# Kernel optimization log

Measured on AMD Instinct MI355X. Metric: run time of the kernel, lower is better.

Reference implementation:

```python
import jax, jax.numpy as jnp
import numpy as np

HIDDEN = 3072
HEADS = 24
HEAD_DIM = HIDDEN // HEADS  # 128
MLP_HIDDEN = 4 * HIDDEN     # 12288
EPS = 1e-6


def rotate_half(x):
    # interleaved pairs: (x1, x2) -> (-x2, x1)
    xr = x.reshape(*x.shape[:-1], -1, 2)
    x1, x2 = xr[..., 0], xr[..., 1]
    return jnp.stack((-x2, x1), axis=-1).reshape(x.shape)


def rms_norm(x, gamma):
    var = jnp.mean(x * x, axis=-1, keepdims=True)
    return x * jax.lax.rsqrt(var + EPS) * gamma


def layer_norm(x):
    mu = jnp.mean(x, axis=-1, keepdims=True)
    var = jnp.mean(jnp.square(x - mu), axis=-1, keepdims=True)
    return (x - mu) * jax.lax.rsqrt(var + EPS)


def setup_inputs() -> dict:
    key = jax.random.key(0)
    ks = jax.random.split(key, 8)
    B, L_IMG, TXT = 2, 1024, 256
    L = L_IMG + TXT
    s = 0.02
    x = jax.random.normal(ks[0], (B, L, HIDDEN), jnp.float32)
    vec = jax.random.normal(ks[1], (B, HIDDEN), jnp.float32)
    w1 = jax.random.normal(ks[2], (HIDDEN, 3 * HIDDEN + MLP_HIDDEN), jnp.float32) * s
    b1 = jnp.zeros((3 * HIDDEN + MLP_HIDDEN,), jnp.float32)
    w2 = jax.random.normal(ks[3], (HIDDEN + MLP_HIDDEN, HIDDEN), jnp.float32) * s
    b2 = jnp.zeros((HIDDEN,), jnp.float32)
    wmod = jax.random.normal(ks[4], (HIDDEN, 3 * HIDDEN), jnp.float32) * s
    bmod = jnp.zeros((3 * HIDDEN,), jnp.float32)
    q_gamma = jnp.ones((HEAD_DIM,), jnp.float32)
    k_gamma = jnp.ones((HEAD_DIM,), jnp.float32)
    # real RoPE tables for the image tokens
    inv_freq = 1.0 / (10000.0 ** (np.arange(0, HEAD_DIM, 2, dtype=np.float32) / HEAD_DIM))
    angles = np.arange(L_IMG, dtype=np.float32)[:, None] * inv_freq[None, :]  # [L_img, D/2]
    freqs_cos = jnp.asarray(np.repeat(np.cos(angles), 2, axis=-1))  # [L_img, D]
    freqs_sin = jnp.asarray(np.repeat(np.sin(angles), 2, axis=-1))
    cu_seqlens_q = jnp.asarray([0, L, L, 2 * L, 2 * L], jnp.int32)  # no padding
    return {"x": x, "vec": vec, "w1": w1, "b1": b1, "w2": w2, "b2": b2,
            "wmod": wmod, "bmod": bmod, "q_gamma": q_gamma, "k_gamma": k_gamma,
            "freqs_cos": freqs_cos, "freqs_sin": freqs_sin,
            "txt_len": TXT, "cu_seqlens_q": cu_seqlens_q}


def reference(x, vec, w1, b1, w2, b2, wmod, bmod, q_gamma, k_gamma,
              freqs_cos, freqs_sin, txt_len, cu_seqlens_q):
    B, L, _ = x.shape
    # modulation: SiLU(vec) @ Wmod -> shift/scale/gate
    mod = jax.nn.silu(vec) @ wmod + bmod              # [B, 3H]
    mod_shift, mod_scale, mod_gate = jnp.split(mod, 3, axis=-1)
    x_mod = layer_norm(x) * (1.0 + mod_scale[:, None, :]) + mod_shift[:, None, :]
    h = x_mod @ w1 + b1                               # [B, L, 3H + mlp]
    qkv, mlp = h[..., :3 * HIDDEN], h[..., 3 * HIDDEN:]
    qkv = qkv.reshape(B, L, 3, HEADS, HEAD_DIM)
    q, k, v = qkv[:, :, 0], qkv[:, :, 1], qkv[:, :, 2]  # [B, L, H, D]
    q = rms_norm(q, q_gamma)
    k = rms_norm(k, k_gamma)
    # RoPE on image tokens (first L - txt_len)
    cos = freqs_cos[None, :, None, :]
    sin = freqs_sin[None, :, None, :]
    img_q, txt_q = q[:, :-txt_len], q[:, -txt_len:]
    img_k, txt_k = k[:, :-txt_len], k[:, -txt_len:]
    img_q = img_q * cos + rotate_half(img_q) * sin
    img_k = img_k * cos + rotate_half(img_k) * sin
    q = jnp.concatenate((img_q, txt_q), axis=1)
    k = jnp.concatenate((img_k, txt_k), axis=1)
    # full attention (no padding => each batch is one varlen segment)
    scale = HEAD_DIM ** -0.5
    scores = jnp.einsum("bqhd,bkhd->bhqk", q, k) * scale
    probs = jax.nn.softmax(scores, axis=-1)
    attn = jnp.einsum("bhqk,bkhd->bqhd", probs, v).reshape(B, L, HIDDEN)
    out = jnp.concatenate((attn, jax.nn.gelu(mlp, approximate=True)), axis=-1) @ w2 + b2
    return x + out * mod_gate[:, None, :]
```

## Files before the change

### kernel.cpp

```cpp
#include <hip/hip_runtime.h>

typedef unsigned short u16;
typedef unsigned int   u32;
typedef __attribute__((ext_vector_type(2))) u16 u16x2;
typedef __attribute__((ext_vector_type(4))) u16 u16x4;
typedef __attribute__((ext_vector_type(8))) u16 u16x8;
typedef __attribute__((ext_vector_type(8))) __bf16 bf16x8;
typedef __attribute__((ext_vector_type(4))) float f32x4;

#define HIDDEN 3072
#define LTOT 1280
#define BATCH 2
#define NROWS (BATCH*LTOT)
#define HEADS 24
#define HD 128
#define N1 21504
#define QKVW 9216
#define MLPW 12288
#define A2W 15360
#define EPSF 1e-6f

__device__ __forceinline__ float b2f(u16 u) {
  union { u32 i; float f; } v; v.i = ((u32)u) << 16; return v.f;
}
__device__ __forceinline__ u16 f2b(float f) {
  union { float f; u32 i; } v; v.f = f;
  u32 r = (v.i + 0x7FFFu + ((v.i >> 16) & 1u)) >> 16;
  return (u16)r;
}
__device__ __forceinline__ float lde(const void* p, size_t i, int f) {
  return f ? b2f(((const u16*)p)[i]) : ((const float*)p)[i];
}
__device__ __forceinline__ void gload16(const void* g, void* l) {
  __builtin_amdgcn_global_load_lds((const __attribute__((address_space(1))) void*)g,
                                   (__attribute__((address_space(3))) void*)l, 16, 0, 0);
}
__device__ __forceinline__ float gelu_tanh(float x) {
  float u = 0.7978845608028654f * (x + 0.044715f * x * x * x);
  float e = __expf(2.0f * u);
  float th = 1.0f - 2.0f / (e + 1.0f);
  return 0.5f * x * (1.0f + th);
}

__global__ void detect_kernel(const u16* __restrict__ fcos, int* __restrict__ dflag) {
  if (threadIdx.x == 0 && blockIdx.x == 0) *dflag = (fcos[0] == 0x3F80) ? 1 : 0;
}

__global__ void silu_kernel(const void* __restrict__ vec, float* __restrict__ sv,
                            const int* __restrict__ dflag) {
  int flag = *dflag;
  int i = blockIdx.x * 256 + threadIdx.x;
  if (i < BATCH * HIDDEN) { float x = lde(vec, i, flag); sv[i] = x / (1.0f + __expf(-x)); }
}

__global__ void modmul(const void* __restrict__ wmod, const float* __restrict__ sv,
                       float* __restrict__ modp, const int* __restrict__ dflag) {
  int flag = *dflag;
  int j = blockIdx.x * 256 + threadIdx.x;
  int kc = blockIdx.y;
  float a = 0.f, c = 0.f;
  int k0 = kc * 384;
  for (int k = k0; k < k0 + 384; ++k) {
    float w = lde(wmod, (size_t)k * QKVW + j, flag);
    a += sv[k] * w; c += sv[HIDDEN + k] * w;
  }
  modp[(size_t)kc * 2 * QKVW + j] = a;
  modp[(size_t)kc * 2 * QKVW + QKVW + j] = c;
}

__global__ void modred(const float* __restrict__ modp, const void* __restrict__ bmod,
                       float* __restrict__ mod, const int* __restrict__ dflag) {
  int flag = *dflag;
  int j = blockIdx.x * 256 + threadIdx.x;
  float bv = lde(bmod, j, flag);
  float a = bv, c = bv;
#pragma unroll
  for (int kc = 0; kc < 8; ++kc) {
    a += modp[(size_t)kc * 2 * QKVW + j];
    c += modp[(size_t)kc * 2 * QKVW + QKVW + j];
  }
  mod[j] = a; mod[QKVW + j] = c;
}

__global__ __launch_bounds__(256) void ln_mod_kernel(const void* __restrict__ x,
                                                     const float* __restrict__ mod,
                                                     u16* __restrict__ xmod,
                                                     const int* __restrict__ dflag) {
  int flag = *dflag;
  int row = blockIdx.x;
  int b = row / LTOT;
  int t = threadIdx.x, w = t >> 6, l = t & 63;
  float v[12], sum = 0.0f, sq = 0.0f;
  if (flag) {
    const u16* xr = (const u16*)x + (size_t)row * HIDDEN;
#pragma unroll
    for (int p = 0; p < 3; ++p) {
      u16x4 u = *(const u16x4*)&xr[p * 1024 + t * 4];
#pragma unroll
      for (int i = 0; i < 4; ++i) { float f = b2f(u[i]); v[p * 4 + i] = f; sum += f; sq += f * f; }
    }
  } else {
    const float* xr = (const float*)x + (size_t)row * HIDDEN;
#pragma unroll
    for (int p = 0; p < 3; ++p) {
      f32x4 u = *(const f32x4*)&xr[p * 1024 + t * 4];
#pragma unroll
      for (int i = 0; i < 4; ++i) { float f = u[i]; v[p * 4 + i] = f; sum += f; sq += f * f; }
    }
  }
#pragma unroll
  for (int off = 1; off < 64; off <<= 1) { sum += __shfl_xor(sum, off, 64); sq += __shfl_xor(sq, off, 64); }
  __shared__ float red[2][4];
  if (l == 0) { red[0][w] = sum; red[1][w] = sq; }
  __syncthreads();
  sum = red[0][0] + red[0][1] + red[0][2] + red[0][3];
  sq  = red[1][0] + red[1][1] + red[1][2] + red[1][3];
  float mu = sum / (float)HIDDEN;
  float var = sq / (float)HIDDEN - mu * mu;
  float rs = rsqrtf(var + EPSF);
  const float* mb = mod + (size_t)b * QKVW;
#pragma unroll
  for (int p = 0; p < 3; ++p) {
    u16x4 o;
#pragma unroll
    for (int i = 0; i < 4; ++i) {
      int col = p * 1024 + t * 4 + i;
      float y = (v[p * 4 + i] - mu) * rs;
      o[i] = f2b(y * (1.0f + mb[HIDDEN + col]) + mb[col]);
    }
    *(u16x4*)&xmod[(size_t)row * HIDDEN + p * 1024 + t * 4] = o;
  }
}

__global__ void transpose_cvt(const void* __restrict__ in, u16* __restrict__ out,
                              int R, int C, const int* __restrict__ dflag) {
  int flag = *dflag;
  __shared__ u16 tile[32][33];
  int bx = blockIdx.x * 32, by = blockIdx.y * 32;
  int tx = threadIdx.x & 31, ty = threadIdx.x >> 5;
#pragma unroll
  for (int i = 0; i < 32; i += 8)
    tile[ty + i][tx] = f2b(lde(in, (size_t)(by + ty + i) * C + bx + tx, flag));
  __syncthreads();
#pragma unroll
  for (int i = 0; i < 32; i += 8) out[(size_t)(bx + ty + i) * R + by + tx] = tile[tx][ty + i];
}

__global__ void transpose_bf16(const u16* __restrict__ in, u16* __restrict__ out,
                               int R, int C, size_t ibs, size_t obs) {
  in  += (size_t)blockIdx.z * ibs;
  out += (size_t)blockIdx.z * obs;
  __shared__ u16 tile[32][33];
  int bx = blockIdx.x * 32, by = blockIdx.y * 32;
  int tx = threadIdx.x & 31, ty = threadIdx.x >> 5;
#pragma unroll
  for (int i = 0; i < 32; i += 8) tile[ty + i][tx] = in[(size_t)(by + ty + i) * C + bx + tx];
  __syncthreads();
#pragma unroll
  for (int i = 0; i < 32; i += 8) out[(size_t)(bx + ty + i) * R + by + tx] = tile[tx][ty + i];
}

template <int MODE>
__global__ __launch_bounds__(256) void gemm_bt(
    const u16* __restrict__ A, const u16* __restrict__ Bt, int K,
    const void* __restrict__ bias,
    u16* __restrict__ out0, u16* __restrict__ out1, u16* __restrict__ out2,
    u16* __restrict__ out3, float* __restrict__ outf,
    const void* __restrict__ xin, const float* __restrict__ mod,
    const int* __restrict__ dflag) {
  __shared__ u16 As[128 * 32];
  __shared__ u16 Bs[128 * 32];
  const int flag = *dflag;
  const int t = threadIdx.x;
  const int bn = blockIdx.x * 128;
  const int bm = blockIdx.y * 128;
  const int w = t >> 6, l = t & 63;
  const int wr = (w >> 1) * 64, wc = (w & 1) * 64;
  const int lr = l & 15, lk = (l >> 4) * 8;
  f32x4 acc[4][4] = {};
  const size_t a_base = (size_t)bm * K;
  const size_t b_base = (size_t)bn * K;
  const int e0 = t * 8, e1 = e0 + 2048;
  const int r0 = e0 >> 5, c0 = e0 & 31;
  const int r1 = e1 >> 5, c1 = e1 & 31;
  const int nk = K / 32;
  for (int kt = 0; kt < nk; ++kt) {
    const int k0 = kt * 32;
    __syncthreads();
    gload16(A + a_base + (size_t)r0 * K + k0 + c0, (u16*)As + e0);
    gload16(A + a_base + (size_t)r1 * K + k0 + c1, (u16*)As + e1);
    gload16(Bt + b_base + (size_t)r0 * K + k0 + c0, (u16*)Bs + e0);
    gload16(Bt + b_base + (size_t)r1 * K + k0 + c1, (u16*)Bs + e1);
    __syncthreads();
    bf16x8 af[4], bfr[4];
#pragma unroll
    for (int i = 0; i < 4; ++i) {
      af[i]  = __builtin_bit_cast(bf16x8, *(const u16x8*)&As[(wr + i * 16 + lr) * 32 + lk]);
      bfr[i] = __builtin_bit_cast(bf16x8, *(const u16x8*)&Bs[(wc + i * 16 + lr) * 32 + lk]);
    }
#pragma unroll
    for (int i = 0; i < 4; ++i)
#pragma unroll
      for (int j = 0; j < 4; ++j)
        acc[i][j] = __builtin_amdgcn_mfma_f32_16x16x32_bf16(af[i], bfr[j], acc[i][j], 0, 0, 0);
  }
#pragma unroll
  for (int i = 0; i < 4; ++i) {
#pragma unroll
    for (int j = 0; j < 4; ++j) {
      int colg = bn + wc + j * 16 + lr;
      float bv = lde(bias, colg, flag);
#pragma unroll
      for (int r = 0; r < 4; ++r) {
        int rowg = bm + wr + i * 16 + (l >> 4) * 4 + r;
        float v = acc[i][j][r] + bv;
        if (MODE == 1) {
          if (colg < QKVW) {
            int which = colg / HIDDEN;
            int hd = colg - which * HIDDEN;
            int h = hd >> 7, d = hd & 127;
            int b = rowg / LTOT, pos = rowg - b * LTOT;
            u16* dst = (which == 0) ? out0 : ((which == 1) ? out1 : out2);
            dst[(((size_t)(b * HEADS + h)) * LTOT + pos) * HD + d] = f2b(v);
          } else {
            out3[(size_t)rowg * A2W + HIDDEN + (colg - QKVW)] = f2b(gelu_tanh(v));
          }
        } else {
          int b = rowg / LTOT;
          float g = mod[(size_t)b * QKVW + 2 * HIDDEN + colg];
          float xv = lde(xin, (size_t)rowg * HIDDEN + colg, flag);
          outf[(size_t)rowg * HIDDEN + colg] = xv + v * g;
        }
      }
    }
  }
}

__global__ __launch_bounds__(256) void rms_rope(
    u16* __restrict__ Qb, u16* __restrict__ Kb,
    const void* __restrict__ qg, const void* __restrict__ kg,
    const void* __restrict__ fcos, const void* __restrict__ fsin,
    const int* __restrict__ dflag) {
  int flag = *dflag;
  int w = threadIdx.x >> 6, l = threadIdx.x & 63;
  int rid = blockIdx.x * 4 + w;
  int pos = rid % LTOT;
  int d0 = 2 * l;
  size_t off = (size_t)rid * HD + d0;
  u16x2 qu = *(const u16x2*)&Qb[off];
  u16x2 ku = *(const u16x2*)&Kb[off];
  float q0 = b2f(qu[0]), q1 = b2f(qu[1]);
  float k0 = b2f(ku[0]), k1 = b2f(ku[1]);
  float sq = q0 * q0 + q1 * q1, sk = k0 * k0 + k1 * k1;
#pragma unroll
  for (int o = 1; o < 64; o <<= 1) { sq += __shfl_xor(sq, o, 64); sk += __shfl_xor(sk, o, 64); }
  float rq = rsqrtf(sq / 128.0f + EPSF), rk = rsqrtf(sk / 128.0f + EPSF);
  q0 *= rq * lde(qg, d0, flag); q1 *= rq * lde(qg, d0 + 1, flag);
  k0 *= rk * lde(kg, d0, flag); k1 *= rk * lde(kg, d0 + 1, flag);
  if (pos < 1024) {
    float cc = lde(fcos, (size_t)pos * HD + d0, flag);
    float ss = lde(fsin, (size_t)pos * HD + d0, flag);
    float nq0 = q0 * cc - q1 * ss, nq1 = q1 * cc + q0 * ss;
    float nk0 = k0 * cc - k1 * ss, nk1 = k1 * cc + k0 * ss;
    q0 = nq0; q1 = nq1; k0 = nk0; k1 = nk1;
  }
  u16x2 qo; qo[0] = f2b(q0); qo[1] = f2b(q1);
  u16x2 ko; ko[0] = f2b(k0); ko[1] = f2b(k1);
  *(u16x2*)&Qb[off] = qo;
  *(u16x2*)&Kb[off] = ko;
}

__global__ __launch_bounds__(256) void attn_kernel(
    const u16* __restrict__ Qb, const u16* __restrict__ Kb, const u16* __restrict__ Vt,
    u16* __restrict__ A2) {
  __shared__ u16 Ks[32 * 128];
  __shared__ u16 Vs[128 * 32];
  __shared__ u16 Ps[4][512];
  int t = threadIdx.x, w = t >> 6, l = t & 63;
  int bh = blockIdx.y;
  int q0 = blockIdx.x * 64 + w * 16;
  size_t base = (size_t)bh * LTOT * HD;
  int lr = l & 15, lk = (l >> 4) * 8;
  const float scale = 0.08838834764831845f;

  bf16x8 qf[4];
#pragma unroll
  for (int c = 0; c < 4; ++c)
    qf[c] = __builtin_bit_cast(bf16x8, *(const u16x8*)&Qb[base + (size_t)(q0 + lr) * HD + c * 32 + lk]);

  f32x4 o[8] = {};
  float mrun[4] = {-1e30f, -1e30f, -1e30f, -1e30f};
  float lrun[4] = {0.f, 0.f, 0.f, 0.f};

  const int e0 = t * 8, e1 = e0 + 2048;
  const int vd0 = e0 >> 5, vc0 = e0 & 31;
  const int vd1 = e1 >> 5, vc1 = e1 & 31;

  for (int kt = 0; kt < LTOT / 32; ++kt) {
    __syncthreads();
    gload16(Kb + base + (size_t)kt * 32 * HD + e0, (u16*)Ks + e0);
    gload16(Kb + base + (size_t)kt * 32 * HD + e1, (u16*)Ks + e1);
    gload16(Vt + base + (size_t)vd0 * LTOT + kt * 32 + vc0, (u16*)Vs + e0);
    gload16(Vt + base + (size_t)vd1 * LTOT + kt * 32 + vc1, (u16*)Vs + e1);
    __syncthreads();

    f32x4 s[2] = {};
#pragma unroll
    for (int sb = 0; sb < 2; ++sb)
#pragma unroll
      for (int c = 0; c < 4; ++c) {
        bf16x8 kf = __builtin_bit_cast(bf16x8, *(const u16x8*)&Ks[(sb * 16 + lr) * 128 + c * 32 + lk]);
        s[sb] = __builtin_amdgcn_mfma_f32_16x16x32_bf16(qf[c], kf, s[sb], 0, 0, 0);
      }
#pragma unroll
    for (int sb = 0; sb < 2; ++sb)
#pragma unroll
      for (int j = 0; j < 4; ++j) s[sb][j] *= scale;

#pragma unroll
    for (int j = 0; j < 4; ++j) {
      float mt = fmaxf(s[0][j], s[1][j]);
#pragma unroll
      for (int off = 1; off < 16; off <<= 1) mt = fmaxf(mt, __shfl_xor(mt, off, 64));
      float mnew = fmaxf(mrun[j], mt);
      float f = __expf(mrun[j] - mnew);
      float p0 = __expf(s[0][j] - mnew), p1 = __expf(s[1][j] - mnew);
      float ps = p0 + p1;
#pragma unroll
      for (int off = 1; off < 16; off <<= 1) ps += __shfl_xor(ps, off, 64);
      lrun[j] = lrun[j] * f + ps;
      mrun[j] = mnew;
#pragma unroll
      for (int nb = 0; nb < 8; ++nb) o[nb][j] *= f;
      int prow = (l >> 4) * 4 + j;
      Ps[w][prow * 32 + lr] = f2b(p0);
      Ps[w][prow * 32 + 16 + lr] = f2b(p1);
    }
    __syncthreads();
    bf16x8 pa = __builtin_bit_cast(bf16x8, *(const u16x8*)&Ps[w][lr * 32 + lk]);
#pragma unroll
    for (int nb = 0; nb < 8; ++nb) {
      bf16x8 vf = __builtin_bit_cast(bf16x8, *(const u16x8*)&Vs[(nb * 16 + lr) * 32 + lk]);
      o[nb] = __builtin_amdgcn_mfma_f32_16x16x32_bf16(pa, vf, o[nb], 0, 0, 0);
    }
  }

  int b = bh / HEADS, h = bh % HEADS;
#pragma unroll
  for (int j = 0; j < 4; ++j) {
    float inv = 1.0f / lrun[j];
    size_t row = (size_t)b * LTOT + q0 + (l >> 4) * 4 + j;
#pragma unroll
    for (int nb = 0; nb < 8; ++nb) {
      int col = h * HD + nb * 16 + lr;
      A2[row * A2W + col] = f2b(o[nb][j] * inv);
    }
  }
}

extern "C" void kernel_launch(void* const* d_in, const int* in_sizes, int n_in,
                              void* d_out, int out_size, void* d_ws, size_t ws_size,
                              hipStream_t stream) {
  const void* x    = d_in[0];
  const void* vec  = d_in[1];
  const void* w1   = d_in[2];
  const void* b1   = d_in[3];
  const void* w2   = d_in[4];
  const void* b2   = d_in[5];
  const void* wmod = d_in[6];
  const void* bmod = d_in[7];
  const void* qg   = d_in[8];
  const void* kg   = d_in[9];
  const void* fcos = d_in[10];
  const void* fsin = d_in[11];

  char* p = (char*)d_ws;
  int* dflag  = (int*)p; p += 256;
  float* sv   = (float*)p; p += 32768;
  float* mod  = (float*)p; p += 131072;
  float* modp = (float*)p; p += 8 * 2 * QKVW * 4;
  u16* xmod = (u16*)p; p += (size_t)NROWS * HIDDEN * 2;
  u16* w1t  = (u16*)p; p += (size_t)N1 * HIDDEN * 2;
  u16* Qb   = (u16*)p; p += (size_t)48 * LTOT * HD * 2;
  u16* Kb   = (u16*)p; p += (size_t)48 * LTOT * HD * 2;
  u16* Vb   = (u16*)p; p += (size_t)48 * LTOT * HD * 2;
  u16* Vt   = (u16*)p; p += (size_t)48 * LTOT * HD * 2;
  u16* A2   = (u16*)p; p += (size_t)NROWS * A2W * 2;
  u16* w2t  = w1t;

  detect_kernel<<<1, 64, 0, stream>>>((const u16*)fcos, dflag);
  silu_kernel<<<24, 256, 0, stream>>>(vec, sv, dflag);
  modmul<<<dim3(36, 8), 256, 0, stream>>>(wmod, sv, modp, dflag);
  modred<<<36, 256, 0, stream>>>(modp, bmod, mod, dflag);
  ln_mod_kernel<<<NROWS, 256, 0, stream>>>(x, mod, xmod, dflag);
  transpose_cvt<<<dim3(N1 / 32, HIDDEN / 32), 256, 0, stream>>>(w1, w1t, HIDDEN, N1, dflag);
  gemm_bt<1><<<dim3(N1 / 128, NROWS / 128), 256, 0, stream>>>(xmod, w1t, HIDDEN, b1,
                                                              Qb, Kb, Vb, A2, nullptr,
                                                              nullptr, nullptr, dflag);
  rms_rope<<<48 * LTOT / 4, 256, 0, stream>>>(Qb, Kb, qg, kg, fcos, fsin, dflag);
  transpose_bf16<<<dim3(HD / 32, LTOT / 32, 48), 256, 0, stream>>>(Vb, Vt, LTOT, HD,
                                                                   (size_t)LTOT * HD, (size_t)LTOT * HD);
  attn_kernel<<<dim3(LTOT / 64, 48), 256, 0, stream>>>(Qb, Kb, Vt, A2);
  transpose_cvt<<<dim3(HIDDEN / 32, A2W / 32), 256, 0, stream>>>(w2, w2t, A2W, HIDDEN, dflag);
  gemm_bt<2><<<dim3(HIDDEN / 128, NROWS / 128), 256, 0, stream>>>(A2, w2t, A2W, b2,
                                                                  nullptr, nullptr, nullptr, nullptr,
                                                                  (float*)d_out, x, mod, dflag);
}
```

Baseline: 1.512 ms.

## Replace first GEMM with 256x256-tile, 512-thread double-buffered swizzled kernel

Adds a dedicated kernel for the large first projection GEMM. It uses 256x256 output tiles with 8 waves and double-buffered LDS filled by direct global-to-LDS loads. Reads use an XOR-swizzled LDS layout to avoid bank conflicts, MFMA sections are raised in priority with s_setprio, and workgroup IDs are remapped across XCDs for better L2 locality. The larger per-wave accumulator tile raises register pressure and cuts the number of workgroups, which risks lower occupancy and tail imbalance. The old MODE 1 epilogue in the generic GEMM is removed.

```diff
diff --git a/kernel.cpp b/kernel.cpp
--- a/kernel.cpp
+++ b/kernel.cpp
@@ -35,6 +35,9 @@
   __builtin_amdgcn_global_load_lds((const __attribute__((address_space(1))) void*)g,
                                    (__attribute__((address_space(3))) void*)l, 16, 0, 0);
 }
+__device__ __forceinline__ bf16x8 ldf(const u16* p) {
+  return __builtin_bit_cast(bf16x8, *(const u16x8*)p);
+}
 __device__ __forceinline__ float gelu_tanh(float x) {
   float u = 0.7978845608028654f * (x + 0.044715f * x * x * x);
   float e = __expf(2.0f * u);
@@ -158,6 +161,127 @@
   __syncthreads();
 #pragma unroll
   for (int i = 0; i < 32; i += 8) out[(size_t)(bx + ty + i) * R + by + tx] = tile[tx][ty + i];
+}
+
+__global__ __launch_bounds__(512, 2) void gemm1_8ph(
+    const u16* __restrict__ A, const u16* __restrict__ Bt,
+    const void* __restrict__ bias,
+    u16* __restrict__ Qb, u16* __restrict__ Kb, u16* __restrict__ Vb,
+    u16* __restrict__ A2, const int* __restrict__ dflag) {
+  __shared__ u16 As[2][2][256][32];
+  __shared__ u16 Bs[2][2][256][32];
+  constexpr int K = HIDDEN;
+  constexpr int NT = K / 64;
+  const int tid = threadIdx.x;
+  const int l = tid & 63, w = tid >> 6;
+  const int wr = w >> 2, wc = w & 3;
+  const int lr = l & 15, g = l >> 4;
+  const int lk_sw = (g ^ ((lr >> 1) & 3)) * 8;
+
+  const int orig = blockIdx.x;
+  const int wgid = (orig & 7) * 105 + (orig >> 3);
+  const int my = wgid / 84, nx = wgid - my * 84;
+  const int bm = my * 256, bn = nx * 256;
+
+  const int row_s = tid >> 2, chunk = tid & 3;
+  const int c_log = chunk ^ ((row_s >> 1) & 3);
+  const u16* pa = A  + (size_t)(bm + row_s) * K + c_log * 8;
+  const u16* pb = Bt + (size_t)(bn + row_s) * K + c_log * 8;
+
+  auto stage = [&](int buf, int kk, int t) {
+    const u16* sa = pa + kk * 32 + t * 64;
+    const u16* sb = pb + kk * 32 + t * 64;
+    u16* la = &As[buf][kk][row_s][chunk * 8];
+    u16* lb = &Bs[buf][kk][row_s][chunk * 8];
+    gload16(sa,                  la);
+    gload16(sa + (size_t)128 * K, la + 128 * 32);
+    gload16(sb,                  lb);
+    gload16(sb + (size_t)128 * K, lb + 128 * 32);
+  };
+
+  f32x4 acc[8][4] = {};
+  stage(0, 0, 0);
+  stage(0, 1, 0);
+
+  for (int t = 0; t < NT; ++t) {
+    const int buf = t & 1;
+    const bool pre = (t + 1 < NT);
+    asm volatile("s_waitcnt vmcnt(4)" ::: "memory");
+    __builtin_amdgcn_s_barrier();
+    __builtin_amdgcn_sched_barrier(0);
+    if (pre) stage(buf ^ 1, 0, t + 1);
+    bf16x8 bfr[4], af[4];
+#pragma unroll
+    for (int fc = 0; fc < 4; ++fc) bfr[fc] = ldf(&Bs[buf][0][wc * 64 + fc * 16 + lr][lk_sw]);
+#pragma unroll
+    for (int j = 0; j < 4; ++j) af[j] = ldf(&As[buf][0][wr * 128 + j * 16 + lr][lk_sw]);
+    __builtin_amdgcn_s_setprio(1);
+#pragma unroll
+    for (int j = 0; j < 4; ++j)
+#pragma unroll
+      for (int fc = 0; fc < 4; ++fc)
+        acc[j][fc] = __builtin_amdgcn_mfma_f32_16x16x32_bf16(af[j], bfr[fc], acc[j][fc], 0, 0, 0);
+    __builtin_amdgcn_s_setprio(0);
+#pragma unroll
+    for (int j = 0; j < 4; ++j) af[j] = ldf(&As[buf][0][wr * 128 + (4 + j) * 16 + lr][lk_sw]);
+    __builtin_amdgcn_s_setprio(1);
+#pragma unroll
+    for (int j = 0; j < 4; ++j)
+#pragma unroll
+      for (int fc = 0; fc < 4; ++fc)
+        acc[4 + j][fc] = __builtin_amdgcn_mfma_f32_16x16x32_bf16(af[j], bfr[fc], acc[4 + j][fc], 0, 0, 0);
+    __builtin_amdgcn_s_setprio(0);
+    if (pre) { asm volatile("s_waitcnt vmcnt(4)" ::: "memory"); }
+    else     { asm volatile("s_waitcnt vmcnt(0)" ::: "memory"); }
+    __builtin_amdgcn_s_barrier();
+    __builtin_amdgcn_sched_barrier(0);
+    if (pre) stage(buf ^ 1, 1, t + 1);
+#pragma unroll
+    for (int fc = 0; fc < 4; ++fc) bfr[fc] = ldf(&Bs[buf][1][wc * 64 + fc * 16 + lr][lk_sw]);
+#pragma unroll
+    for (int j = 0; j < 4; ++j) af[j] = ldf(&As[buf][1][wr * 128 + j * 16 + lr][lk_sw]);
+    __builtin_amdgcn_s_setprio(1);
+#pragma unroll
+    for (int j = 0; j < 4; ++j)
+#pragma unroll
+      for (int fc = 0; fc < 4; ++fc)
+        acc[j][fc] = __builtin_amdgcn_mfma_f32_16x16x32_bf16(af[j], bfr[fc], acc[j][fc], 0, 0, 0);
+    __builtin_amdgcn_s_setprio(0);
+#pragma unroll
+    for (int j = 0; j < 4; ++j) af[j] = ldf(&As[buf][1][wr * 128 + (4 + j) * 16 + lr][lk_sw]);
+    __builtin_amdgcn_s_setprio(1);
+#pragma unroll
+    for (int j = 0; j < 4; ++j)
+#pragma unroll
+      for (int fc = 0; fc < 4; ++fc)
+        acc[4 + j][fc] = __builtin_amdgcn_mfma_f32_16x16x32_bf16(af[j], bfr[fc], acc[4 + j][fc], 0, 0, 0);
+    __builtin_amdgcn_s_setprio(0);
+  }
+
+  const int flag = *dflag;
+#pragma unroll
+  for (int fr = 0; fr < 8; ++fr) {
+#pragma unroll
+    for (int fc = 0; fc < 4; ++fc) {
+      int colg = bn + wc * 64 + fc * 16 + lr;
+      float bv = lde(bias, colg, flag);
+#pragma unroll
+      for (int r = 0; r < 4; ++r) {
+        int rowg = bm + wr * 128 + fr * 16 + g * 4 + r;
+        float v = acc[fr][fc][r] + bv;
+        if (colg < QKVW) {
+          int which = colg / HIDDEN;
+          int hd = colg - which * HIDDEN;
+          int h = hd >> 7, d = hd & 127;
+          int b = rowg / LTOT, pos = rowg - b * LTOT;
+          u16* dst = (which == 0) ? Qb : ((which == 1) ? Kb : Vb);
+          dst[(((size_t)(b * HEADS + h)) * LTOT + pos) * HD + d] = f2b(v);
+        } else {
+          A2[(size_t)rowg * A2W + HIDDEN + (colg - QKVW)] = f2b(gelu_tanh(v));
+        }
+      }
+    }
+  }
 }
 
 template <int MODE>
@@ -215,21 +339,11 @@
         int rowg = bm + wr + i * 16 + (l >> 4) * 4 + r;
         float v = acc[i][j][r] + bv;
         if (MODE == 1) {
-          if (colg < QKVW) {
-            int which = colg / HIDDEN;
-            int hd = colg - which * HIDDEN;
-            int h = hd >> 7, d = hd & 127;
-            int b = rowg / LTOT, pos = rowg - b * LTOT;
-            u16* dst = (which == 0) ? out0 : ((which == 1) ? out1 : out2);
-            dst[(((size_t)(b * HEADS + h)) * LTOT + pos) * HD + d] = f2b(v);
-          } else {
-            out3[(size_t)rowg * A2W + HIDDEN + (colg - QKVW)] = f2b(gelu_tanh(v));
-          }
         } else {
           int b = rowg / LTOT;
-          float g = mod[(size_t)b * QKVW + 2 * HIDDEN + colg];
+          float gg = mod[(size_t)b * QKVW + 2 * HIDDEN + colg];
           float xv = lde(xin, (size_t)rowg * HIDDEN + colg, flag);
-          outf[(size_t)rowg * HIDDEN + colg] = xv + v * g;
+          outf[(size_t)rowg * HIDDEN + colg] = xv + v * gg;
         }
       }
     }
@@ -394,9 +508,8 @@
   modred<<<36, 256, 0, stream>>>(modp, bmod, mod, dflag);
   ln_mod_kernel<<<NROWS, 256, 0, stream>>>(x, mod, xmod, dflag);
   transpose_cvt<<<dim3(N1 / 32, HIDDEN / 32), 256, 0, stream>>>(w1, w1t, HIDDEN, N1, dflag);
-  gemm_bt<1><<<dim3(N1 / 128, NROWS / 128), 256, 0, stream>>>(xmod, w1t, HIDDEN, b1,
-                                                              Qb, Kb, Vb, A2, nullptr,
-                                                              nullptr, nullptr, dflag);
+  gemm1_8ph<<<(N1 / 256) * (NROWS / 256), 512, 0, stream>>>(xmod, w1t, b1,
+                                                            Qb, Kb, Vb, A2, dflag);
   rms_rope<<<48 * LTOT / 4, 256, 0, stream>>>(Qb, Kb, qg, kg, fcos, fsin, dflag);
   transpose_bf16<<<dim3(HD / 32, LTOT / 32, 48), 256, 0, stream>>>(Vb, Vt, LTOT, HD,
                                                                    (size_t)LTOT * HD, (size_t)LTOT * HD);
```

Measured after the change: 1.539 ms, median of 5. Within noise of the previous version (+1.8%).
